# Kernel optimization log

Measured on AMD Instinct MI355X. Metric: run time of the kernel, lower is better.

## Reference

```python
import jax, jax.numpy as jnp
import numpy as np

D = 16          # manifold_dim
M = 8192        # mem_slots
H = 256         # slot_dim
K_BASE = 32     # topk
K_BIG = 48      # int(K_BASE * 1.5), used when internal lightbulb fires
INPUT_DIM = 1024
ODE_HID = 128
ODE_STEPS = 2
ODE_DT = 0.5
TEMPERATURE = 1.0      # buffer initial value
LB_TOP1_AVG = 1.0      # buffer initial value
LB_DROP_RATIO = 0.7
BIG = 1e30


def layer_norm(x, g, b, eps=1e-5):
    mu = jnp.mean(x, axis=-1, keepdims=True)
    var = jnp.mean(jnp.square(x - mu), axis=-1, keepdims=True)
    return (x - mu) * jax.lax.rsqrt(var + eps) * g + b


def setup_inputs() -> dict:
    key = jax.random.key(0)
    ks = jax.random.split(key, 12)
    B, S = 4, 2048
    T3 = D * 3
    s_in = 1.0 / np.sqrt(INPUT_DIM)
    s_3d = 1.0 / np.sqrt(T3)
    s_h = 1.0 / np.sqrt(H)
    s_ode = 1.0 / np.sqrt(ODE_HID)
    return {
        "x": jax.random.normal(ks[0], (B, S, INPUT_DIM), jnp.float32),
        "W_proj": jax.random.normal(ks[1], (INPUT_DIM, T3), jnp.float32) * s_in,
        "b_proj": jnp.zeros((T3,), jnp.float32),
        "ln1_g": jnp.ones((T3,), jnp.float32),
        "ln1_b": jnp.zeros((T3,), jnp.float32),
        "ode_W1": jax.random.normal(ks[2], (T3, ODE_HID), jnp.float32) * s_3d,
        "ode_b1": jnp.zeros((ODE_HID,), jnp.float32),
        "ode_W2": jax.random.normal(ks[3], (ODE_HID, T3), jnp.float32) * s_ode,
        "ode_b2": jnp.zeros((T3,), jnp.float32),
        "memory_slots": jax.random.normal(ks[4], (M, H), jnp.float32),
        "pos_enc": jax.random.normal(ks[5], (M, D, 3), jnp.float32),
        "curvature": jax.random.normal(ks[6], (M, D), jnp.float32),
        "curv_alpha": jnp.float32(0.1),
        "W_out": jax.random.normal(ks[7], (H, INPUT_DIM), jnp.float32) * s_h,
        "b_out": jnp.zeros((INPUT_DIM,), jnp.float32),
        "ln2_g": jnp.ones((INPUT_DIM,), jnp.float32),
        "ln2_b": jnp.zeros((INPUT_DIM,), jnp.float32),
    }


def reference(x, W_proj, b_proj, ln1_g, ln1_b, ode_W1, ode_b1, ode_W2, ode_b2,
              memory_slots, pos_enc, curvature, curv_alpha, W_out, b_out, ln2_g, ln2_b):
    # manifold projection: Linear -> LayerNorm -> GELU   (B,S,3D)
    h = jax.nn.gelu(layer_norm(x @ W_proj + b_proj, ln1_g, ln1_b), approximate=False)
    # ODE evolution (2 steps): x + dt * MLP(x), operating on flattened (B,S,3D)
    for _ in range(ODE_STEPS):
        dh = jnp.tanh(h @ ode_W1 + ode_b1) @ ode_W2 + ode_b2
        h = h + ODE_DT * dh
    # _attend: query positions are detached in the original
    q = jax.lax.stop_gradient(h)                       # (B,S,3D)
    mem_pos = pos_enc.reshape(M, D * 3)                # (M,3D)
    # fast pairwise squared-L2 distance: ||q||^2 + ||m||^2 - 2 q.m
    q2 = jnp.sum(q * q, axis=-1, keepdims=True)        # (B,S,1)
    m2 = jnp.sum(mem_pos * mem_pos, axis=-1)           # (M,)
    dist = jnp.maximum(q2 + m2 - 2.0 * jnp.einsum('bsd,md->bsm', q, mem_pos), 0.0)
    dist = dist / max(TEMPERATURE, 1e-6)
    curv_w = jnp.exp(-curv_alpha * jnp.linalg.norm(curvature, axis=-1))  # (M,)
    dist = dist * curv_w                               # (B,S,M)
    # dynamic top-K: take K_BIG smallest, mask down to K_BASE if lightbulb not fired
    neg_vals, itop = jax.lax.top_k(-dist, K_BIG)       # smallest K_BIG distances
    dtop = -neg_vals                                    # ascending (B,S,K_BIG)
    top1 = jnp.mean(dtop[..., 0])
    internal_fire = top1 < LB_DROP_RATIO * LB_TOP1_AVG
    keep = jnp.logical_or(internal_fire, jnp.arange(K_BIG) < K_BASE)  # (K_BIG,)
    d_eff = jnp.where(keep, dtop, BIG)
    w = jax.nn.softmax(-d_eff, axis=-1)                # (B,S,K_BIG)
    mem = memory_slots[itop]                           # gather (B,S,K_BIG,H)
    attended = jnp.einsum('bsk,bskh->bsh', w, mem)     # (B,S,H)
    out = jax.nn.gelu(layer_norm(attended @ W_out + b_out, ln2_g, ln2_b), approximate=False)
    return out
```

## Files before the change

kernel.cpp:

```cpp
#include <hip/hip_runtime.h>
#include <math.h>

#define NQ    8192
#define T3    48
#define INDIM 1024
#define HID   128
#define MSLOT 8192
#define HD    256
#define KBIG  48
#define KBASE 32
#define NSAMP 1024
#define NTIL  32
#define TCAP  48
#define RSTR  (NTIL * TCAP)

#define OFF_QH    ((size_t)0)
#define OFF_QL    ((size_t)1048576)
#define OFF_Q2    ((size_t)2097152)
#define OFF_M2    ((size_t)2129920)
#define OFF_CW    ((size_t)2162688)
#define OFF_TOPV  ((size_t)2195456)
#define OFF_TOPI  ((size_t)3768320)
#define OFF_RMIN  ((size_t)5341184)
#define OFF_FLAG  ((size_t)5373952)
#define OFF_WOT   ((size_t)5374208)
#define OFF_PEH   ((size_t)5898496)
#define OFF_PEL   ((size_t)6947072)
#define OFF_WPTH  ((size_t)7995648)
#define OFF_WPTL  ((size_t)8093952)
#define OFF_H0    ((size_t)8192256)
#define OFF_RTHR  ((size_t)9765120)
#define OFF_ATTB  ((size_t)9830656)
#define OFF_DISTS ((size_t)14024960)
#define OFF_CANDS ((size_t)47579392)
#define OFF_CNT2  ((size_t)150994944)

typedef __attribute__((ext_vector_type(8))) short short8;
typedef __attribute__((ext_vector_type(4))) float f32x4;

__device__ __forceinline__ float gelu_exact(float x) {
    return 0.5f * x * (1.0f + erff(x * 0.70710678118654752f));
}

__device__ __forceinline__ unsigned short bf16_rne(float f) {
    unsigned int x = __float_as_uint(f);
    unsigned int r = (x + 0x7fffu + ((x >> 16) & 1u)) >> 16;
    return (unsigned short)r;
}

__device__ __forceinline__ void split2(float x, unsigned short& h, unsigned short& l) {
    h = bf16_rne(x);
    l = bf16_rne(x - __uint_as_float((unsigned)h << 16));
}

__global__ __launch_bounds__(256) void k0_prep(const float* __restrict__ pe,
        const float* __restrict__ curv, const float* __restrict__ alpha,
        float* __restrict__ m2, float* __restrict__ cw,
        unsigned short* __restrict__ ph, unsigned short* __restrict__ pl) {
    int m = blockIdx.x * 256 + threadIdx.x;
    float s = 0.f;
    for (int d = 0; d < T3; d++) { float v = pe[(size_t)m * T3 + d]; s += v * v; }
    m2[m] = s;
    float c = 0.f;
    for (int d = 0; d < 16; d++) { float v = curv[m * 16 + d]; c += v * v; }
    cw[m] = expf(-alpha[0] * sqrtf(c));
    int base = blockIdx.x * 256;
    for (int idx = threadIdx.x; idx < 256 * 64; idx += 256) {
        int r = idx >> 6, cc = idx & 63;
        unsigned short hi = 0, lo = 0;
        if (cc < T3) split2(pe[(size_t)(base + r) * T3 + cc], hi, lo);
        size_t o = (size_t)(base + r) * 64 + cc;
        ph[o] = hi; pl[o] = lo;
    }
}

__global__ __launch_bounds__(256) void k0b_cvt(const float* __restrict__ Wo,
        unsigned short* __restrict__ Wot) {
    __shared__ float t[64][65];
    int k0 = blockIdx.x * 64;
    int n0 = blockIdx.y * 64;
    int c = threadIdx.x & 63, r4 = threadIdx.x >> 6;
    #pragma unroll
    for (int i = 0; i < 16; i++) {
        int kr = i * 4 + r4;
        t[kr][c] = Wo[(size_t)(k0 + kr) * INDIM + n0 + c];
    }
    __syncthreads();
    #pragma unroll
    for (int i = 0; i < 16; i++) {
        int nr = i * 4 + r4;
        Wot[(size_t)(n0 + nr) * HD + k0 + c] = bf16_rne(t[c][nr]);
    }
}

__global__ __launch_bounds__(256) void k0d_wpt(const float* __restrict__ Wp,
        unsigned short* __restrict__ wph, unsigned short* __restrict__ wpl) {
    int n = blockIdx.x;
    for (int k = threadIdx.x; k < INDIM; k += 256) {
        unsigned short h, l;
        split2(Wp[(size_t)k * T3 + n], h, l);
        wph[(size_t)n * INDIM + k] = h;
        wpl[(size_t)n * INDIM + k] = l;
    }
}

__global__ __launch_bounds__(256) void k1_mfma(const float* __restrict__ x,
        const unsigned short* __restrict__ wph, const unsigned short* __restrict__ wpl,
        float* __restrict__ h0) {
    __shared__ float part[4][16][48];
    int tid = threadIdx.x, lane = tid & 63, wv = tid >> 6;
    int r0 = blockIdx.x * 16;
    int lm = lane & 15, lk8 = (lane >> 4) * 8;
    f32x4 acc[3];
    #pragma unroll
    for (int j = 0; j < 3; j++) acc[j] = (f32x4)(0.f);
    int kw = wv * 256;
    for (int ks = 0; ks < 8; ks++) {
        int kofs = kw + ks * 32 + lk8;
        short8 ah, al, bh[3], bl[3];
        {
            const float* xp = x + (size_t)(r0 + lm) * INDIM + kofs;
            float4 xa = *(const float4*)xp;
            float4 xb = *(const float4*)(xp + 4);
            float va[8] = {xa.x, xa.y, xa.z, xa.w, xb.x, xb.y, xb.z, xb.w};
            #pragma unroll
            for (int e = 0; e < 8; e++) {
                unsigned short h, l;
                split2(va[e], h, l);
                ah[e] = (short)h; al[e] = (short)l;
            }
        }
        #pragma unroll
        for (int j = 0; j < 3; j++) {
            size_t bo = (size_t)(j * 16 + lm) * INDIM + kofs;
            bh[j] = *(const short8*)(wph + bo);
            bl[j] = *(const short8*)(wpl + bo);
        }
        #pragma unroll
        for (int j = 0; j < 3; j++) {
            f32x4 a = acc[j];
            a = __builtin_amdgcn_mfma_f32_16x16x32_bf16(ah, bh[j], a, 0, 0, 0);
            a = __builtin_amdgcn_mfma_f32_16x16x32_bf16(ah, bl[j], a, 0, 0, 0);
            a = __builtin_amdgcn_mfma_f32_16x16x32_bf16(al, bh[j], a, 0, 0, 0);
            acc[j] = a;
        }
    }
    int orow = (lane >> 4) * 4;
    #pragma unroll
    for (int j = 0; j < 3; j++)
        #pragma unroll
        for (int r = 0; r < 4; r++)
            part[wv][orow + r][j * 16 + lm] = acc[j][r];
    __syncthreads();
    for (int idx = tid; idx < 16 * 48; idx += 256) {
        int rr = idx / 48, cc = idx - rr * 48;
        float s = part[0][rr][cc] + part[1][rr][cc] + part[2][rr][cc] + part[3][rr][cc];
        h0[(size_t)(r0 + rr) * T3 + cc] = s;
    }
}

__global__ __launch_bounds__(256) void k1b_ode(const float* __restrict__ h0,
        const float* __restrict__ bp,
        const float* __restrict__ g1, const float* __restrict__ b1ln,
        const float* __restrict__ W1, const float* __restrict__ bb1,
        const float* __restrict__ W2, const float* __restrict__ bb2,
        unsigned short* __restrict__ qh, unsigned short* __restrict__ ql,
        float* __restrict__ q2out) {
    __shared__ __align__(16) float W1s[T3 * HID];
    __shared__ __align__(16) float W2s[HID * T3];
    __shared__ __align__(16) float hs[16 * T3];
    __shared__ __align__(16) float t1s[16 * 132];
    int tid = threadIdx.x;
    size_t base = (size_t)blockIdx.x * 16 * T3;
    for (int i = tid; i < 1536; i += 256) {
        *(float4*)&W1s[i * 4] = *(const float4*)&W1[i * 4];
        *(float4*)&W2s[i * 4] = *(const float4*)&W2[i * 4];
    }
    for (int idx = tid; idx < 16 * T3; idx += 256) {
        int c = idx % T3;
        t1s[idx] = bp[c] + h0[base + idx];
    }
    __syncthreads();
    {
        int r = tid >> 4, c16 = tid & 15;
        float v[3];
        float ssum = 0.f;
        #pragma unroll
        for (int i = 0; i < 3; i++) { v[i] = t1s[r * T3 + c16 * 3 + i]; ssum += v[i]; }
        #pragma unroll
        for (int off = 1; off < 16; off <<= 1) ssum += __shfl_xor(ssum, off);
        float mean = ssum * (1.f / T3);
        float vv = 0.f;
        #pragma unroll
        for (int i = 0; i < 3; i++) { v[i] -= mean; vv += v[i] * v[i]; }
        #pragma unroll
        for (int off = 1; off < 16; off <<= 1) vv += __shfl_xor(vv, off);
        float rstd = rsqrtf(vv * (1.f / T3) + 1e-5f);
        #pragma unroll
        for (int i = 0; i < 3; i++) {
            int c = c16 * 3 + i;
            hs[r * T3 + c] = gelu_exact(v[i] * rstd * g1[c] + b1ln[c]);
        }
    }
    __syncthreads();
    for (int step = 0; step < 2; step++) {
        #pragma unroll
        for (int it = 0; it < 2; it++) {
            int idx = tid + it * 256;
            int rr = idx >> 5, j4 = idx & 31;
            float4 a = *(const float4*)&bb1[j4 * 4];
            #pragma unroll 3
            for (int d4 = 0; d4 < 12; d4++) {
                float4 qv = *(const float4*)&hs[rr * T3 + d4 * 4];
                float qa[4] = {qv.x, qv.y, qv.z, qv.w};
                #pragma unroll
                for (int dd = 0; dd < 4; dd++) {
                    float4 wv = *(const float4*)&W1s[(d4 * 4 + dd) * HID + j4 * 4];
                    a.x += qa[dd] * wv.x; a.y += qa[dd] * wv.y;
                    a.z += qa[dd] * wv.z; a.w += qa[dd] * wv.w;
                }
            }
            a.x = tanhf(a.x); a.y = tanhf(a.y); a.z = tanhf(a.z); a.w = tanhf(a.w);
            *(float4*)&t1s[rr * 132 + j4 * 4] = a;
        }
        __syncthreads();
        if (tid < 192) {
            int rr = tid / 12, c4 = tid % 12;
            float4 a = *(const float4*)&bb2[c4 * 4];
            #pragma unroll 4
            for (int j4 = 0; j4 < 32; j4++) {
                float4 tv = *(const float4*)&t1s[rr * 132 + j4 * 4];
                float ta[4] = {tv.x, tv.y, tv.z, tv.w};
                #pragma unroll
                for (int jj = 0; jj < 4; jj++) {
                    float4 wv = *(const float4*)&W2s[(j4 * 4 + jj) * T3 + c4 * 4];
                    a.x += ta[jj] * wv.x; a.y += ta[jj] * wv.y;
                    a.z += ta[jj] * wv.z; a.w += ta[jj] * wv.w;
                }
            }
            float4 cur = *(const float4*)&hs[rr * T3 + c4 * 4];
            cur.x += 0.5f * a.x; cur.y += 0.5f * a.y;
            cur.z += 0.5f * a.z; cur.w += 0.5f * a.w;
            *(float4*)&hs[rr * T3 + c4 * 4] = cur;
        }
        __syncthreads();
    }
    {
        int r = tid >> 4, c16 = tid & 15;
        float sq = 0.f;
        #pragma unroll
        for (int i = 0; i < 3; i++) { float v = hs[r * T3 + c16 * 3 + i]; sq += v * v; }
        #pragma unroll
        for (int off = 1; off < 16; off <<= 1) sq += __shfl_xor(sq, off);
        if (c16 == 0) q2out[(size_t)blockIdx.x * 16 + r] = sq;
    }
    for (int idx = tid; idx < 16 * 64; idx += 256) {
        int r = idx >> 6, c = idx & 63;
        unsigned short hi = 0, lo = 0;
        if (c < T3) split2(hs[r * T3 + c], hi, lo);
        size_t o = ((size_t)blockIdx.x * 16 + r) * 64 + c;
        qh[o] = hi; ql[o] = lo;
    }
}

#define PES 72
__global__ __launch_bounds__(256, 4) void k2a_mfma(
        const unsigned short* __restrict__ qh, const unsigned short* __restrict__ ql,
        const float* __restrict__ q2g,
        const unsigned short* __restrict__ ph, const unsigned short* __restrict__ pl,
        const float* __restrict__ m2, const float* __restrict__ cw,
        float* __restrict__ dist, int rowstride) {
    __shared__ __align__(16) char smem[256 * PES * 2];
    __shared__ float q2s[32];
    unsigned short* pesh = (unsigned short*)smem;
    int tid = threadIdx.x, lane = tid & 63, wv = tid >> 6;
    int c0 = blockIdx.x * 256;
    int grow0 = blockIdx.y * 32;
    for (int idx = tid; idx < 2048; idx += 256) {
        int col = idx >> 3, ch = idx & 7;
        *(uint4*)&pesh[col * PES + ch * 8] = *(const uint4*)&ph[(size_t)(c0 + col) * 64 + ch * 8];
    }
    if (tid < 32) q2s[tid] = q2g[grow0 + tid];
    int lm = lane & 15, lk8 = (lane >> 4) * 8;
    int mco = wv * 64;
    short8 bqh[2][2], bql[2][2];
    #pragma unroll
    for (int qs = 0; qs < 2; qs++)
        #pragma unroll
        for (int ks = 0; ks < 2; ks++) {
            size_t o = (size_t)(grow0 + qs * 16 + lm) * 64 + ks * 32 + lk8;
            bqh[qs][ks] = *(const short8*)&qh[o];
            bql[qs][ks] = *(const short8*)&ql[o];
        }
    short8 al0[4], al1[4];
    #pragma unroll
    for (int ms = 0; ms < 4; ms++) {
        size_t plo = (size_t)(c0 + mco + ms * 16 + lm) * 64;
        al0[ms] = *(const short8*)&pl[plo + lk8];
        al1[ms] = *(const short8*)&pl[plo + 32 + lk8];
    }
    __syncthreads();
    f32x4 acc[4][2];
    #pragma unroll
    for (int i = 0; i < 4; i++)
        #pragma unroll
        for (int j = 0; j < 2; j++) acc[i][j] = (f32x4)(0.f);
    #pragma unroll
    for (int ms = 0; ms < 4; ms++) {
        int arow = mco + ms * 16 + lm;
        short8 ah0 = *(const short8*)&pesh[arow * PES + lk8];
        short8 ah1 = *(const short8*)&pesh[arow * PES + 32 + lk8];
        #pragma unroll
        for (int qs = 0; qs < 2; qs++) {
            f32x4 a = acc[ms][qs];
            a = __builtin_amdgcn_mfma_f32_16x16x32_bf16(ah0, bqh[qs][0], a, 0, 0, 0);
            a = __builtin_amdgcn_mfma_f32_16x16x32_bf16(ah1, bqh[qs][1], a, 0, 0, 0);
            a = __builtin_amdgcn_mfma_f32_16x16x32_bf16(ah0, bql[qs][0], a, 0, 0, 0);
            a = __builtin_amdgcn_mfma_f32_16x16x32_bf16(ah1, bql[qs][1], a, 0, 0, 0);
            a = __builtin_amdgcn_mfma_f32_16x16x32_bf16(al0[ms], bqh[qs][0], a, 0, 0, 0);
            a = __builtin_amdgcn_mfma_f32_16x16x32_bf16(al1[ms], bqh[qs][1], a, 0, 0, 0);
            acc[ms][qs] = a;
        }
    }
    int mr4 = (lane >> 4) * 4;
    #pragma unroll
    for (int ms = 0; ms < 4; ms++) {
        int gm = c0 + mco + ms * 16 + mr4;
        float4 m2v = *(const float4*)&m2[gm];
        float4 cwv = *(const float4*)&cw[gm];
        float m2a[4] = {m2v.x, m2v.y, m2v.z, m2v.w};
        float cwa[4] = {cwv.x, cwv.y, cwv.z, cwv.w};
        #pragma unroll
        for (int qs = 0; qs < 2; qs++) {
            float q2 = q2s[qs * 16 + lm];
            #pragma unroll
            for (int c = 0; c < 4; c++)
                acc[ms][qs][c] = fmaxf(q2 + m2a[c] - 2.f * acc[ms][qs][c], 0.f) * cwa[c];
        }
    }
    __syncthreads();
    float (*dt)[260] = (float(*)[260])smem;
    #pragma unroll
    for (int ms = 0; ms < 4; ms++)
        #pragma unroll
        for (int qs = 0; qs < 2; qs++) {
            float4 o;
            o.x = acc[ms][qs][0]; o.y = acc[ms][qs][1];
            o.z = acc[ms][qs][2]; o.w = acc[ms][qs][3];
            *(float4*)&dt[qs * 16 + lm][mco + ms * 16 + mr4] = o;
        }
    __syncthreads();
    #pragma unroll
    for (int i = 0; i < 8; i++) {
        int qrow = wv * 8 + i;
        float4 v = *(const float4*)&dt[qrow][lane * 4];
        *(float4*)&dist[(size_t)(grow0 + qrow) * rowstride + c0 + lane * 4] = v;
    }
}

#define NBINT 2048
#define MAXCT 512
__global__ __launch_bounds__(256) void k2b_thr(const float* __restrict__ dists,
        float* __restrict__ rowthr) {
    __shared__ unsigned int hist[NBINT];
    __shared__ unsigned long long cand[MAXCT];
    __shared__ float s_wmin[4], s_wmax[4];
    __shared__ unsigned int wsum[4];
    __shared__ unsigned int s_B, s_ncand;
    int tid = threadIdx.x, lane = tid & 63, wv = tid >> 6;
    int row = blockIdx.x;
    float4 v4 = *(const float4*)(dists + (size_t)row * NSAMP + tid * 4);
    float fv[4] = {v4.x, v4.y, v4.z, v4.w};
    float mn = fminf(fminf(fv[0], fv[1]), fminf(fv[2], fv[3]));
    float mx = fmaxf(fmaxf(fv[0], fv[1]), fmaxf(fv[2], fv[3]));
    #pragma unroll
    for (int off = 32; off; off >>= 1) {
        mn = fminf(mn, __shfl_xor(mn, off));
        mx = fmaxf(mx, __shfl_xor(mx, off));
    }
    if (lane == 0) { s_wmin[wv] = mn; s_wmax[wv] = mx; }
    __syncthreads();
    float m0 = fminf(fminf(s_wmin[0], s_wmin[1]), fminf(s_wmin[2], s_wmin[3]));
    float mX = fmaxf(fmaxf(s_wmax[0], s_wmax[1]), fmaxf(s_wmax[2], s_wmax[3]));
    float lo = m0;
    float width = fmaxf(m0 * 0.5f, 1e-3f);
    float fullw = fmaxf((mX - m0) * 1.0001f, 1e-3f) + 1e-6f;
    unsigned B = 0;
    float scale = 0.f, hiT = 0.f;
    for (int att = 0; att < 7; att++) {
        if (att == 6 || width > fullw) width = fullw;
        hiT = lo + width;
        scale = (float)NBINT / width;
        for (int i = tid; i < NBINT; i += 256) hist[i] = 0;
        __syncthreads();
        #pragma unroll
        for (int j = 0; j < 4; j++) {
            float v = fv[j];
            if (v < hiT) {
                int b = (int)((v - lo) * scale);
                b = b < NBINT - 1 ? b : NBINT - 1;
                atomicAdd(&hist[b], 1u);
            }
        }
        __syncthreads();
        unsigned hb[8];
        unsigned s = 0;
        #pragma unroll
        for (int i = 0; i < 8; i++) { hb[i] = hist[tid * 8 + i]; s += hb[i]; }
        unsigned v = s;
        #pragma unroll
        for (int off = 1; off < 64; off <<= 1) {
            unsigned o = __shfl_up(v, off);
            if (lane >= off) v += o;
        }
        if (lane == 63) wsum[wv] = v;
        __syncthreads();
        unsigned wbase = 0;
        for (int w = 0; w < wv; w++) wbase += wsum[w];
        unsigned total = wsum[0] + wsum[1] + wsum[2] + wsum[3];
        if (total >= KBIG) {
            unsigned excl = wbase + v - s;
            if (excl < KBIG && KBIG <= excl + s) {
                unsigned c = excl;
                #pragma unroll
                for (int i = 0; i < 8; i++) {
                    if (c < KBIG && KBIG <= c + hb[i]) { s_B = tid * 8 + i; break; }
                    c += hb[i];
                }
            }
            __syncthreads();
            B = s_B;
            break;
        }
        width *= 8.f;
        __syncthreads();
    }
    if (tid == 0) s_ncand = 0;
    __syncthreads();
    #pragma unroll
    for (int j = 0; j < 4; j++) {
        float v = fv[j];
        if (v < hiT) {
            int b = (int)((v - lo) * scale);
            b = b < NBINT - 1 ? b : NBINT - 1;
            if ((unsigned)b <= B) {
                unsigned n = atomicAdd(&s_ncand, 1u);
                if (n < MAXCT)
                    cand[n] = ((unsigned long long)__float_as_uint(v) << 32)
                              | (unsigned)(tid * 4 + j);
            }
        }
    }
    __syncthreads();
    int nc = (int)(s_ncand < MAXCT ? s_ncand : MAXCT);
    for (int i = tid; i < nc; i += 256) {
        unsigned long long me = cand[i];
        int rank = 0;
        for (int j = 0; j < nc; j++) rank += (cand[j] < me) ? 1 : 0;
        if (rank == KBIG - 1)
            rowthr[row] = __uint_as_float((unsigned)(me >> 32));
    }
}

__global__ __launch_bounds__(256, 4) void k2c_filter(
        const unsigned short* __restrict__ qh, const unsigned short* __restrict__ ql,
        const float* __restrict__ q2g,
        const unsigned short* __restrict__ ph, const unsigned short* __restrict__ pl,
        const float* __restrict__ m2, const float* __restrict__ cw,
        const float* __restrict__ rowthr, int* __restrict__ cnt2,
        unsigned long long* __restrict__ cands) {
    __shared__ __align__(16) char smem[256 * PES * 2];
    __shared__ float q2s[32];
    __shared__ float thrs[32];
    __shared__ unsigned int lcnt[32];
    unsigned short* pesh = (unsigned short*)smem;
    int tid = threadIdx.x, lane = tid & 63, wv = tid >> 6;
    int tile = blockIdx.x;
    int c0 = tile * 256;
    int grow0 = blockIdx.y * 32;
    for (int idx = tid; idx < 2048; idx += 256) {
        int col = idx >> 3, ch = idx & 7;
        *(uint4*)&pesh[col * PES + ch * 8] = *(const uint4*)&ph[(size_t)(c0 + col) * 64 + ch * 8];
    }
    if (tid < 32) {
        q2s[tid] = q2g[grow0 + tid];
        thrs[tid] = rowthr[grow0 + tid];
        lcnt[tid] = 0;
    }
    int lm = lane & 15, lk8 = (lane >> 4) * 8;
    int mco = wv * 64;
    short8 bqh[2][2], bql[2][2];
    #pragma unroll
    for (int qs = 0; qs < 2; qs++)
        #pragma unroll
        for (int ks = 0; ks < 2; ks++) {
            size_t o = (size_t)(grow0 + qs * 16 + lm) * 64 + ks * 32 + lk8;
            bqh[qs][ks] = *(const short8*)&qh[o];
            bql[qs][ks] = *(const short8*)&ql[o];
        }
    short8 al0[4], al1[4];
    #pragma unroll
    for (int ms = 0; ms < 4; ms++) {
        size_t plo = (size_t)(c0 + mco + ms * 16 + lm) * 64;
        al0[ms] = *(const short8*)&pl[plo + lk8];
        al1[ms] = *(const short8*)&pl[plo + 32 + lk8];
    }
    __syncthreads();
    f32x4 acc[4][2];
    #pragma unroll
    for (int i = 0; i < 4; i++)
        #pragma unroll
        for (int j = 0; j < 2; j++) acc[i][j] = (f32x4)(0.f);
    #pragma unroll
    for (int ms = 0; ms < 4; ms++) {
        int arow = mco + ms * 16 + lm;
        short8 ah0 = *(const short8*)&pesh[arow * PES + lk8];
        short8 ah1 = *(const short8*)&pesh[arow * PES + 32 + lk8];
        #pragma unroll
        for (int qs = 0; qs < 2; qs++) {
            f32x4 a = acc[ms][qs];
            a = __builtin_amdgcn_mfma_f32_16x16x32_bf16(ah0, bqh[qs][0], a, 0, 0, 0);
            a = __builtin_amdgcn_mfma_f32_16x16x32_bf16(ah1, bqh[qs][1], a, 0, 0, 0);
            a = __builtin_amdgcn_mfma_f32_16x16x32_bf16(ah0, bql[qs][0], a, 0, 0, 0);
            a = __builtin_amdgcn_mfma_f32_16x16x32_bf16(ah1, bql[qs][1], a, 0, 0, 0);
            a = __builtin_amdgcn_mfma_f32_16x16x32_bf16(al0[ms], bqh[qs][0], a, 0, 0, 0);
            a = __builtin_amdgcn_mfma_f32_16x16x32_bf16(al1[ms], bqh[qs][1], a, 0, 0, 0);
            acc[ms][qs] = a;
        }
    }
    int mr4 = (lane >> 4) * 4;
    #pragma unroll
    for (int ms = 0; ms < 4; ms++) {
        int gm = c0 + mco + ms * 16 + mr4;
        float4 m2v = *(const float4*)&m2[gm];
        float4 cwv = *(const float4*)&cw[gm];
        float m2a[4] = {m2v.x, m2v.y, m2v.z, m2v.w};
        float cwa[4] = {cwv.x, cwv.y, cwv.z, cwv.w};
        #pragma unroll
        for (int qs = 0; qs < 2; qs++) {
            float q2 = q2s[qs * 16 + lm];
            #pragma unroll
            for (int c = 0; c < 4; c++)
                acc[ms][qs][c] = fmaxf(q2 + m2a[c] - 2.f * acc[ms][qs][c], 0.f) * cwa[c];
        }
    }
    __syncthreads();
    unsigned long long (*lbuf)[TCAP] = (unsigned long long(*)[TCAP])smem;
    #pragma unroll
    for (int ms = 0; ms < 4; ms++) {
        int gm = c0 + mco + ms * 16 + mr4;
        #pragma unroll
        for (int qs = 0; qs < 2; qs++) {
            int q = qs * 16 + lm;
            float thr = thrs[q];
            #pragma unroll
            for (int c = 0; c < 4; c++) {
                float v = acc[ms][qs][c];
                if (v <= thr) {
                    unsigned slot = atomicAdd(&lcnt[q], 1u);
                    if (slot < TCAP)
                        lbuf[q][slot] = ((unsigned long long)__float_as_uint(v) << 32)
                                        | (unsigned)(gm + c);
                }
            }
        }
    }
    __syncthreads();
    if (tid < 32) {
        unsigned k = lcnt[tid];
        k = k < TCAP ? k : TCAP;
        lcnt[tid] = k;
        cnt2[(size_t)(grow0 + tid) * NTIL + tile] = (int)k;
    }
    __syncthreads();
    for (int idx = tid; idx < 32 * TCAP; idx += 256) {
        int q = idx / TCAP, i = idx - q * TCAP;
        if (i < (int)lcnt[q])
            cands[(size_t)(grow0 + q) * RSTR + tile * TCAP + i] = lbuf[q][i];
    }
}

#define NBIND 2048
#define FINCAP 512
#define CLCAP (NTIL * TCAP)
__global__ __launch_bounds__(256) void k2d_select(
        const unsigned long long* __restrict__ cands, const int* __restrict__ cnt2,
        float* __restrict__ topv, int* __restrict__ topi, float* __restrict__ rowmin) {
    __shared__ unsigned long long cl[CLCAP];
    __shared__ unsigned int hist[NBIND];
    __shared__ unsigned long long fin[FINCAP];
    __shared__ int cnt2s[NTIL];
    __shared__ float s_mn[4], s_mx[4];
    __shared__ unsigned int wsum[4];
    __shared__ unsigned int s_B, s_nc, s_nfin;
    int tid = threadIdx.x, lane = tid & 63, wv = tid >> 6;
    size_t row = blockIdx.x;
    if (tid < NTIL) cnt2s[tid] = cnt2[row * NTIL + tid];
    for (int i = tid; i < NBIND; i += 256) hist[i] = 0;
    if (tid == 0) { s_nc = 0; s_nfin = 0; }
    __syncthreads();
    for (int idx = tid; idx < CLCAP; idx += 256) {
        int t = idx / TCAP, i = idx - t * TCAP;
        if (i < cnt2s[t]) {
            unsigned n = atomicAdd(&s_nc, 1u);
            cl[n] = cands[row * RSTR + idx];
        }
    }
    __syncthreads();
    int nc = (int)s_nc;
    float mn = 3.4e38f, mx = -3.4e38f;
    for (int i = tid; i < nc; i += 256) {
        float v = __uint_as_float((unsigned)(cl[i] >> 32));
        mn = fminf(mn, v); mx = fmaxf(mx, v);
    }
    #pragma unroll
    for (int off = 32; off; off >>= 1) {
        mn = fminf(mn, __shfl_xor(mn, off));
        mx = fmaxf(mx, __shfl_xor(mx, off));
    }
    if (lane == 0) { s_mn[wv] = mn; s_mx[wv] = mx; }
    __syncthreads();
    float m0 = fminf(fminf(s_mn[0], s_mn[1]), fminf(s_mn[2], s_mn[3]));
    float mX = fmaxf(fmaxf(s_mx[0], s_mx[1]), fmaxf(s_mx[2], s_mx[3]));
    float width = fmaxf((mX - m0) * 1.0001f, 1e-9f) + 1e-12f;
    float scale = (float)NBIND / width;
    for (int i = tid; i < nc; i += 256) {
        float v = __uint_as_float((unsigned)(cl[i] >> 32));
        int b = (int)((v - m0) * scale);
        b = b < NBIND - 1 ? b : NBIND - 1;
        atomicAdd(&hist[b], 1u);
    }
    __syncthreads();
    {
        unsigned hb[8];
        unsigned s = 0;
        #pragma unroll
        for (int i = 0; i < 8; i++) { hb[i] = hist[tid * 8 + i]; s += hb[i]; }
        unsigned v = s;
        #pragma unroll
        for (int off = 1; off < 64; off <<= 1) {
            unsigned o = __shfl_up(v, off);
            if (lane >= off) v += o;
        }
        if (lane == 63) wsum[wv] = v;
        __syncthreads();
        unsigned wbase = 0;
        for (int w = 0; w < wv; w++) wbase += wsum[w];
        unsigned excl = wbase + v - s;
        unsigned tgt = (unsigned)(nc < KBIG ? nc : KBIG);
        if (excl < tgt && tgt <= excl + s) {
            unsigned c = excl;
            #pragma unroll
            for (int i = 0; i < 8; i++) {
                if (c < tgt && tgt <= c + hb[i]) { s_B = tid * 8 + i; break; }
                c += hb[i];
            }
        }
        __syncthreads();
    }
    unsigned B = s_B;
    for (int i = tid; i < nc; i += 256) {
        float v = __uint_as_float((unsigned)(cl[i] >> 32));
        int b = (int)((v - m0) * scale);
        b = b < NBIND - 1 ? b : NBIND - 1;
        if ((unsigned)b <= B) {
            unsigned n = atomicAdd(&s_nfin, 1u);
            if (n < FINCAP) fin[n] = cl[i];
        }
    }
    __syncthreads();
    int nf = (int)s_nfin;
    if (nf <= FINCAP) {
        for (int i = tid; i < nf; i += 256) {
            unsigned long long me = fin[i];
            int rank = 0;
            for (int j = 0; j < nf; j++) rank += (fin[j] < me) ? 1 : 0;
            if (rank < KBIG) {
                float v = __uint_as_float((unsigned)(me >> 32));
                topv[row * KBIG + rank] = v;
                topi[row * KBIG + rank] = (int)(me & 0xFFFFFFFFu);
                if (rank == 0) rowmin[row] = v;
            }
        }
    } else {
        for (int i = tid; i < nc; i += 256) {
            unsigned long long me = cl[i];
            int rank = 0;
            for (int j = 0; j < nc; j++) rank += (cl[j] < me) ? 1 : 0;
            if (rank < KBIG) {
                float v = __uint_as_float((unsigned)(me >> 32));
                topv[row * KBIG + rank] = v;
                topi[row * KBIG + rank] = (int)(me & 0xFFFFFFFFu);
                if (rank == 0) rowmin[row] = v;
            }
        }
    }
}

__global__ __launch_bounds__(256) void k3a_flag(const float* __restrict__ rowmin,
        int* __restrict__ flag) {
    __shared__ float red[256];
    int tid = threadIdx.x;
    float s = 0.f;
    for (int j = 0; j < NQ / 256; j++) s += rowmin[tid + 256 * j];
    red[tid] = s;
    __syncthreads();
    for (int st = 128; st; st >>= 1) {
        if (tid < st) red[tid] += red[tid + st];
        __syncthreads();
    }
    if (tid == 0) {
        float top1 = red[0] / (float)NQ;
        flag[0] = (top1 < 0.7f) ? 1 : 0;
    }
}

__global__ __launch_bounds__(256) void k3_attend(const float* __restrict__ topv,
        const int* __restrict__ topi, const int* __restrict__ flag,
        const float* __restrict__ slots, unsigned short* __restrict__ attb) {
    int tid = threadIdx.x;
    int lane = tid & 63, wv = tid >> 6;
    size_t row = (size_t)blockIdx.x * 4 + wv;
    int kc = flag[0] ? KBIG : KBASE;
    float v0 = topv[row * KBIG];
    float ev = 0.f;
    int mi = 0;
    if (lane < KBIG) {
        float v = topv[row * KBIG + lane];
        ev = (lane < kc) ? expf(-(v - v0)) : 0.f;
        mi = topi[row * KBIG + lane];
    }
    float ssum = ev;
    #pragma unroll
    for (int off = 32; off; off >>= 1) ssum += __shfl_xor(ssum, off);
    float inv = 1.f / ssum;
    float4 acc = make_float4(0.f, 0.f, 0.f, 0.f);
    for (int k = 0; k < kc; k++) {
        float wk = __shfl(ev, k) * inv;
        int m = __shfl(mi, k);
        float4 v = *(const float4*)(slots + (size_t)m * HD + lane * 4);
        acc.x += wk * v.x; acc.y += wk * v.y;
        acc.z += wk * v.z; acc.w += wk * v.w;
    }
    ushort4 o;
    o.x = bf16_rne(acc.x); o.y = bf16_rne(acc.y);
    o.z = bf16_rne(acc.z); o.w = bf16_rne(acc.w);
    *(ushort4*)(attb + row * HD + lane * 4) = o;
}

__global__ __launch_bounds__(256) void k4_mfma(const unsigned short* __restrict__ A,
        const unsigned short* __restrict__ Bt, const float* __restrict__ bo,
        float* __restrict__ out) {
    int tid = threadIdx.x;
    int lane = tid & 63, wave = tid >> 6;
    int wm = wave >> 1, wn = wave & 1;
    int mbase = blockIdx.y * 128 + wm * 64;
    int nbase = blockIdx.x * 128 + wn * 64;
    int lm = lane & 15;
    int lk8 = (lane >> 4) * 8;
    f32x4 acc[4][4];
    #pragma unroll
    for (int i = 0; i < 4; i++)
        #pragma unroll
        for (int j = 0; j < 4; j++) acc[i][j] = (f32x4)(0.f);
    #pragma unroll 2
    for (int ks = 0; ks < 8; ks++) {
        int kofs = ks * 32 + lk8;
        short8 a[4], b[4];
        #pragma unroll
        for (int i = 0; i < 4; i++)
            a[i] = *(const short8*)(A + (size_t)(mbase + i * 16 + lm) * HD + kofs);
        #pragma unroll
        for (int j = 0; j < 4; j++)
            b[j] = *(const short8*)(Bt + (size_t)(nbase + j * 16 + lm) * HD + kofs);
        #pragma unroll
        for (int i = 0; i < 4; i++)
            #pragma unroll
            for (int j = 0; j < 4; j++)
                acc[i][j] = __builtin_amdgcn_mfma_f32_16x16x32_bf16(a[i], b[j], acc[i][j], 0, 0, 0);
    }
    int orow = (lane >> 4) * 4;
    #pragma unroll
    for (int i = 0; i < 4; i++)
        #pragma unroll
        for (int j = 0; j < 4; j++) {
            int col = nbase + j * 16 + lm;
            float bias = bo[col];
            #pragma unroll
            for (int r = 0; r < 4; r++) {
                int row = mbase + i * 16 + orow + r;
                out[(size_t)row * INDIM + col] = acc[i][j][r] + bias;
            }
        }
}

__global__ __launch_bounds__(256) void k5_ln(float* __restrict__ out,
        const float* __restrict__ g, const float* __restrict__ b) {
    __shared__ float red[4];
    int tid = threadIdx.x;
    size_t row = blockIdx.x;
    float4 v = *(const float4*)(out + row * INDIM + tid * 4);
    float s = v.x + v.y + v.z + v.w;
    #pragma unroll
    for (int off = 32; off; off >>= 1) s += __shfl_xor(s, off);
    int wid = tid >> 6, lane = tid & 63;
    if (!lane) red[wid] = s;
    __syncthreads();
    float mean = (red[0] + red[1] + red[2] + red[3]) * (1.f / (float)INDIM);
    __syncthreads();
    float dx = v.x - mean, dy = v.y - mean, dz = v.z - mean, dw = v.w - mean;
    float ss = dx * dx + dy * dy + dz * dz + dw * dw;
    #pragma unroll
    for (int off = 32; off; off >>= 1) ss += __shfl_xor(ss, off);
    if (!lane) red[wid] = ss;
    __syncthreads();
    float var = (red[0] + red[1] + red[2] + red[3]) * (1.f / (float)INDIM);
    float rs = rsqrtf(var + 1e-5f);
    int c = tid * 4;
    float4 o;
    o.x = gelu_exact(dx * rs * g[c + 0] + b[c + 0]);
    o.y = gelu_exact(dy * rs * g[c + 1] + b[c + 1]);
    o.z = gelu_exact(dz * rs * g[c + 2] + b[c + 2]);
    o.w = gelu_exact(dw * rs * g[c + 3] + b[c + 3]);
    *(float4*)(out + row * INDIM + c) = o;
}

extern "C" void kernel_launch(void* const* d_in, const int* in_sizes, int n_in,
                              void* d_out, int out_size, void* d_ws, size_t ws_size,
                              hipStream_t stream) {
    const float* x     = (const float*)d_in[0];
    const float* Wp    = (const float*)d_in[1];
    const float* bp    = (const float*)d_in[2];
    const float* ln1g  = (const float*)d_in[3];
    const float* ln1b  = (const float*)d_in[4];
    const float* oW1   = (const float*)d_in[5];
    const float* ob1   = (const float*)d_in[6];
    const float* oW2   = (const float*)d_in[7];
    const float* ob2   = (const float*)d_in[8];
    const float* slots = (const float*)d_in[9];
    const float* pe    = (const float*)d_in[10];
    const float* curv  = (const float*)d_in[11];
    const float* alpha = (const float*)d_in[12];
    const float* Wo    = (const float*)d_in[13];
    const float* bo    = (const float*)d_in[14];
    const float* ln2g  = (const float*)d_in[15];
    const float* ln2b  = (const float*)d_in[16];
    float* out = (float*)d_out;
    char* ws = (char*)d_ws;

    unsigned short* qhp = (unsigned short*)(ws + OFF_QH);
    unsigned short* qlp = (unsigned short*)(ws + OFF_QL);
    float* q2p    = (float*)(ws + OFF_Q2);
    float* m2     = (float*)(ws + OFF_M2);
    float* cwv    = (float*)(ws + OFF_CW);
    float* topv   = (float*)(ws + OFF_TOPV);
    int*   topi   = (int*)  (ws + OFF_TOPI);
    float* rowmin = (float*)(ws + OFF_RMIN);
    int*   flag   = (int*)  (ws + OFF_FLAG);
    unsigned short* wot  = (unsigned short*)(ws + OFF_WOT);
    unsigned short* peh  = (unsigned short*)(ws + OFF_PEH);
    unsigned short* pel  = (unsigned short*)(ws + OFF_PEL);
    unsigned short* wpth = (unsigned short*)(ws + OFF_WPTH);
    unsigned short* wptl = (unsigned short*)(ws + OFF_WPTL);
    float* h0     = (float*)(ws + OFF_H0);
    float* rowthr = (float*)(ws + OFF_RTHR);
    unsigned short* attb = (unsigned short*)(ws + OFF_ATTB);
    float* dists  = (float*)(ws + OFF_DISTS);
    unsigned long long* cands = (unsigned long long*)(ws + OFF_CANDS);
    int*   cnt2   = (int*)  (ws + OFF_CNT2);

    k0_prep<<<MSLOT / 256, 256, 0, stream>>>(pe, curv, alpha, m2, cwv, peh, pel);
    k0b_cvt<<<dim3(4, 16), 256, 0, stream>>>(Wo, wot);
    k0d_wpt<<<T3, 256, 0, stream>>>(Wp, wpth, wptl);
    k1_mfma<<<NQ / 16, 256, 0, stream>>>(x, wpth, wptl, h0);
    k1b_ode<<<NQ / 16, 256, 0, stream>>>(h0, bp, ln1g, ln1b, oW1, ob1, oW2, ob2,
                                         qhp, qlp, q2p);
    k2a_mfma<<<dim3(NSAMP / 256, NQ / 32), 256, 0, stream>>>(
        qhp, qlp, q2p, peh, pel, m2, cwv, dists, NSAMP);
    k2b_thr<<<NQ, 256, 0, stream>>>(dists, rowthr);
    k2c_filter<<<dim3(NTIL, NQ / 32), 256, 0, stream>>>(
        qhp, qlp, q2p, peh, pel, m2, cwv, rowthr, cnt2, cands);
    k2d_select<<<NQ, 256, 0, stream>>>(cands, cnt2, topv, topi, rowmin);
    k3a_flag<<<1, 256, 0, stream>>>(rowmin, flag);
    k3_attend<<<NQ / 4, 256, 0, stream>>>(topv, topi, flag, slots, attb);
    k4_mfma<<<dim3(INDIM / 128, NQ / 128), 256, 0, stream>>>(attb, wot, bo, out);
    k5_ln<<<NQ, 256, 0, stream>>>(out, ln2g, ln2b);
}
```

Measured before the change: 281.1 us.

## Reuse staged memory tile across eight query groups in filter; prefix-sum candidate compaction

The filter kernel now loops over 8 groups of 32 query rows per block, so the 256-slot position tile in shared memory, the low-part registers and the m2/curvature weights are loaded once and reused rather than reloaded for every 32-row block. The grid shrinks by 8x in the row dimension and occupancy hint drops to 3 because separate shared buffers and more live registers are needed. The select kernel replaces the atomic-counter compaction of candidates with a wave prefix sum over per-tile counts, giving deterministic ordering and fewer shared atomics. The risk is fewer blocks for latency hiding and extra barriers per group.

```diff
diff --git a/kernel.cpp b/kernel.cpp
--- a/kernel.cpp
+++ b/kernel.cpp
@@ -13,6 +13,7 @@
 #define NTIL  32
 #define TCAP  48
 #define RSTR  (NTIL * TCAP)
+#define MROW  8
 
 #define OFF_QH    ((size_t)0)
 #define OFF_QL    ((size_t)1048576)
@@ -462,42 +463,30 @@
     }
 }
 
-__global__ __launch_bounds__(256, 4) void k2c_filter(
+__global__ __launch_bounds__(256, 3) void k2c_filter(
         const unsigned short* __restrict__ qh, const unsigned short* __restrict__ ql,
         const float* __restrict__ q2g,
         const unsigned short* __restrict__ ph, const unsigned short* __restrict__ pl,
         const float* __restrict__ m2, const float* __restrict__ cw,
         const float* __restrict__ rowthr, int* __restrict__ cnt2,
         unsigned long long* __restrict__ cands) {
-    __shared__ __align__(16) char smem[256 * PES * 2];
-    __shared__ float q2s[32];
-    __shared__ float thrs[32];
+    __shared__ __align__(16) unsigned short pesh[256 * PES];
+    __shared__ unsigned long long lbuf[32][TCAP];
+    __shared__ float q2a[256];
+    __shared__ float thra[256];
     __shared__ unsigned int lcnt[32];
-    unsigned short* pesh = (unsigned short*)smem;
     int tid = threadIdx.x, lane = tid & 63, wv = tid >> 6;
     int tile = blockIdx.x;
     int c0 = tile * 256;
-    int grow0 = blockIdx.y * 32;
+    int rb0 = blockIdx.y * 256;
     for (int idx = tid; idx < 2048; idx += 256) {
         int col = idx >> 3, ch = idx & 7;
         *(uint4*)&pesh[col * PES + ch * 8] = *(const uint4*)&ph[(size_t)(c0 + col) * 64 + ch * 8];
     }
-    if (tid < 32) {
-        q2s[tid] = q2g[grow0 + tid];
-        thrs[tid] = rowthr[grow0 + tid];
-        lcnt[tid] = 0;
-    }
+    q2a[tid] = q2g[rb0 + tid];
+    thra[tid] = rowthr[rb0 + tid];
     int lm = lane & 15, lk8 = (lane >> 4) * 8;
     int mco = wv * 64;
-    short8 bqh[2][2], bql[2][2];
-    #pragma unroll
-    for (int qs = 0; qs < 2; qs++)
-        #pragma unroll
-        for (int ks = 0; ks < 2; ks++) {
-            size_t o = (size_t)(grow0 + qs * 16 + lm) * 64 + ks * 32 + lk8;
-            bqh[qs][ks] = *(const short8*)&qh[o];
-            bql[qs][ks] = *(const short8*)&ql[o];
-        }
     short8 al0[4], al1[4];
     #pragma unroll
     for (int ms = 0; ms < 4; ms++) {
@@ -505,78 +494,84 @@
         al0[ms] = *(const short8*)&pl[plo + lk8];
         al1[ms] = *(const short8*)&pl[plo + 32 + lk8];
     }
-    __syncthreads();
-    f32x4 acc[4][2];
-    #pragma unroll
-    for (int i = 0; i < 4; i++)
-        #pragma unroll
-        for (int j = 0; j < 2; j++) acc[i][j] = (f32x4)(0.f);
-    #pragma unroll
-    for (int ms = 0; ms < 4; ms++) {
-        int arow = mco + ms * 16 + lm;
-        short8 ah0 = *(const short8*)&pesh[arow * PES + lk8];
-        short8 ah1 = *(const short8*)&pesh[arow * PES + 32 + lk8];
-        #pragma unroll
-        for (int qs = 0; qs < 2; qs++) {
-            f32x4 a = acc[ms][qs];
-            a = __builtin_amdgcn_mfma_f32_16x16x32_bf16(ah0, bqh[qs][0], a, 0, 0, 0);
-            a = __builtin_amdgcn_mfma_f32_16x16x32_bf16(ah1, bqh[qs][1], a, 0, 0, 0);
-            a = __builtin_amdgcn_mfma_f32_16x16x32_bf16(ah0, bql[qs][0], a, 0, 0, 0);
-            a = __builtin_amdgcn_mfma_f32_16x16x32_bf16(ah1, bql[qs][1], a, 0, 0, 0);
-            a = __builtin_amdgcn_mfma_f32_16x16x32_bf16(al0[ms], bqh[qs][0], a, 0, 0, 0);
-            a = __builtin_amdgcn_mfma_f32_16x16x32_bf16(al1[ms], bqh[qs][1], a, 0, 0, 0);
-            acc[ms][qs] = a;
-        }
-    }
     int mr4 = (lane >> 4) * 4;
+    float m2a[4][4], cwa[4][4];
     #pragma unroll
     for (int ms = 0; ms < 4; ms++) {
         int gm = c0 + mco + ms * 16 + mr4;
         float4 m2v = *(const float4*)&m2[gm];
         float4 cwv = *(const float4*)&cw[gm];
-        float m2a[4] = {m2v.x, m2v.y, m2v.z, m2v.w};
-        float cwa[4] = {cwv.x, cwv.y, cwv.z, cwv.w};
-        #pragma unroll
-        for (int qs = 0; qs < 2; qs++) {
-            float q2 = q2s[qs * 16 + lm];
+        m2a[ms][0] = m2v.x; m2a[ms][1] = m2v.y; m2a[ms][2] = m2v.z; m2a[ms][3] = m2v.w;
+        cwa[ms][0] = cwv.x; cwa[ms][1] = cwv.y; cwa[ms][2] = cwv.z; cwa[ms][3] = cwv.w;
+    }
+    for (int g = 0; g < MROW; g++) {
+        int grow0 = rb0 + g * 32;
+        short8 bqh[2][2], bql[2][2];
+        #pragma unroll
+        for (int qs = 0; qs < 2; qs++)
             #pragma unroll
-            for (int c = 0; c < 4; c++)
-                acc[ms][qs][c] = fmaxf(q2 + m2a[c] - 2.f * acc[ms][qs][c], 0.f) * cwa[c];
-        }
-    }
-    __syncthreads();
-    unsigned long long (*lbuf)[TCAP] = (unsigned long long(*)[TCAP])smem;
-    #pragma unroll
-    for (int ms = 0; ms < 4; ms++) {
-        int gm = c0 + mco + ms * 16 + mr4;
-        #pragma unroll
-        for (int qs = 0; qs < 2; qs++) {
-            int q = qs * 16 + lm;
-            float thr = thrs[q];
+            for (int ks = 0; ks < 2; ks++) {
+                size_t o = (size_t)(grow0 + qs * 16 + lm) * 64 + ks * 32 + lk8;
+                bqh[qs][ks] = *(const short8*)&qh[o];
+                bql[qs][ks] = *(const short8*)&ql[o];
+            }
+        if (tid < 32) lcnt[tid] = 0;
+        __syncthreads();
+        f32x4 acc[4][2];
+        #pragma unroll
+        for (int i = 0; i < 4; i++)
             #pragma unroll
-            for (int c = 0; c < 4; c++) {
-                float v = acc[ms][qs][c];
-                if (v <= thr) {
-                    unsigned slot = atomicAdd(&lcnt[q], 1u);
-                    if (slot < TCAP)
-                        lbuf[q][slot] = ((unsigned long long)__float_as_uint(v) << 32)
-                                        | (unsigned)(gm + c);
+            for (int j = 0; j < 2; j++) acc[i][j] = (f32x4)(0.f);
+        #pragma unroll
+        for (int ms = 0; ms < 4; ms++) {
+            int arow = mco + ms * 16 + lm;
+            short8 ah0 = *(const short8*)&pesh[arow * PES + lk8];
+            short8 ah1 = *(const short8*)&pesh[arow * PES + 32 + lk8];
+            #pragma unroll
+            for (int qs = 0; qs < 2; qs++) {
+                f32x4 a = acc[ms][qs];
+                a = __builtin_amdgcn_mfma_f32_16x16x32_bf16(ah0, bqh[qs][0], a, 0, 0, 0);
+                a = __builtin_amdgcn_mfma_f32_16x16x32_bf16(ah1, bqh[qs][1], a, 0, 0, 0);
+                a = __builtin_amdgcn_mfma_f32_16x16x32_bf16(ah0, bql[qs][0], a, 0, 0, 0);
+                a = __builtin_amdgcn_mfma_f32_16x16x32_bf16(ah1, bql[qs][1], a, 0, 0, 0);
+                a = __builtin_amdgcn_mfma_f32_16x16x32_bf16(al0[ms], bqh[qs][0], a, 0, 0, 0);
+                a = __builtin_amdgcn_mfma_f32_16x16x32_bf16(al1[ms], bqh[qs][1], a, 0, 0, 0);
+                acc[ms][qs] = a;
+            }
+        }
+        #pragma unroll
+        for (int ms = 0; ms < 4; ms++) {
+            int gm = c0 + mco + ms * 16 + mr4;
+            #pragma unroll
+            for (int qs = 0; qs < 2; qs++) {
+                int q = qs * 16 + lm;
+                float q2 = q2a[g * 32 + q];
+                float thr = thra[g * 32 + q];
+                #pragma unroll
+                for (int c = 0; c < 4; c++) {
+                    float v = fmaxf(q2 + m2a[ms][c] - 2.f * acc[ms][qs][c], 0.f) * cwa[ms][c];
+                    if (v <= thr) {
+                        unsigned slot = atomicAdd(&lcnt[q], 1u);
+                        if (slot < TCAP)
+                            lbuf[q][slot] = ((unsigned long long)__float_as_uint(v) << 32)
+                                            | (unsigned)(gm + c);
+                    }
                 }
             }
         }
-    }
-    __syncthreads();
-    if (tid < 32) {
-        unsigned k = lcnt[tid];
-        k = k < TCAP ? k : TCAP;
-        lcnt[tid] = k;
-        cnt2[(size_t)(grow0 + tid) * NTIL + tile] = (int)k;
-    }
-    __syncthreads();
-    for (int idx = tid; idx < 32 * TCAP; idx += 256) {
-        int q = idx / TCAP, i = idx - q * TCAP;
-        if (i < (int)lcnt[q])
-            cands[(size_t)(grow0 + q) * RSTR + tile * TCAP + i] = lbuf[q][i];
+        __syncthreads();
+        if (tid < 32) {
+            unsigned k = lcnt[tid];
+            k = k < TCAP ? k : TCAP;
+            lcnt[tid] = k;
+            cnt2[(size_t)(grow0 + tid) * NTIL + tile] = (int)k;
+        }
+        __syncthreads();
+        for (int idx = tid; idx < 32 * TCAP; idx += 256) {
+            int q = idx / TCAP, i = idx - q * TCAP;
+            if (i < (int)lcnt[q])
+                cands[(size_t)(grow0 + q) * RSTR + tile * TCAP + i] = lbuf[q][i];
+        }
     }
 }
 
@@ -590,24 +585,34 @@
     __shared__ unsigned int hist[NBIND];
     __shared__ unsigned long long fin[FINCAP];
     __shared__ int cnt2s[NTIL];
+    __shared__ int offs[NTIL];
+    __shared__ int s_nc;
     __shared__ float s_mn[4], s_mx[4];
     __shared__ unsigned int wsum[4];
-    __shared__ unsigned int s_B, s_nc, s_nfin;
+    __shared__ unsigned int s_B, s_nfin;
     int tid = threadIdx.x, lane = tid & 63, wv = tid >> 6;
     size_t row = blockIdx.x;
     if (tid < NTIL) cnt2s[tid] = cnt2[row * NTIL + tid];
     for (int i = tid; i < NBIND; i += 256) hist[i] = 0;
-    if (tid == 0) { s_nc = 0; s_nfin = 0; }
-    __syncthreads();
+    if (tid == 0) s_nfin = 0;
+    __syncthreads();
+    if (tid < 64) {
+        int v = (lane < NTIL) ? cnt2s[lane] : 0;
+        #pragma unroll
+        for (int off = 1; off < 32; off <<= 1) {
+            int o = __shfl_up(v, off);
+            if (lane >= off) v += o;
+        }
+        if (lane < NTIL) offs[lane] = v - cnt2s[lane];
+        if (lane == NTIL - 1) s_nc = v;
+    }
+    __syncthreads();
+    int nc = s_nc;
     for (int idx = tid; idx < CLCAP; idx += 256) {
         int t = idx / TCAP, i = idx - t * TCAP;
-        if (i < cnt2s[t]) {
-            unsigned n = atomicAdd(&s_nc, 1u);
-            cl[n] = cands[row * RSTR + idx];
-        }
-    }
-    __syncthreads();
-    int nc = (int)s_nc;
+        if (i < cnt2s[t]) cl[offs[t] + i] = cands[row * RSTR + idx];
+    }
+    __syncthreads();
     float mn = 3.4e38f, mx = -3.4e38f;
     for (int i = tid; i < nc; i += 256) {
         float v = __uint_as_float((unsigned)(cl[i] >> 32));
@@ -878,7 +883,7 @@
     k2a_mfma<<<dim3(NSAMP / 256, NQ / 32), 256, 0, stream>>>(
         qhp, qlp, q2p, peh, pel, m2, cwv, dists, NSAMP);
     k2b_thr<<<NQ, 256, 0, stream>>>(dists, rowthr);
-    k2c_filter<<<dim3(NTIL, NQ / 32), 256, 0, stream>>>(
+    k2c_filter<<<dim3(NTIL, NQ / 256), 256, 0, stream>>>(
         qhp, qlp, q2p, peh, pel, m2, cwv, rowthr, cnt2, cands);
     k2d_select<<<NQ, 256, 0, stream>>>(cands, cnt2, topv, topi, rowmin);
     k3a_flag<<<1, 256, 0, stream>>>(rowmin, flag);
```

After: 282.3 us. About the same (+0.4%).
